# Performance work log

Hardware: AMD Instinct MI355X
Metric: run time of the kernel (lower is better)

Reference implementation:

```python
import jax, jax.numpy as jnp
import numpy as np


def _local_conv2d(x, w, b):
    """Untied (locally connected) conv, stride 1, VALID.
    x: (B, C, H, W); w: (1, O, C, Ho, Wo, k*k); b: (1, O, Ho, Wo) or None.
    Matches torch: x.unfold(2,k).unfold(3,k) -> (B,C,Ho,Wo,k,k) flattened (k*k),
    then (x[:,None] * w).sum([2,-1]) + b.
    """
    B, C, H, W = x.shape
    Ho, Wo = w.shape[3], w.shape[4]
    kh = H - Ho + 1
    kw = W - Wo + 1
    # patches: (B, C*kh*kw, Ho, Wo), feature dim ordered (C, kh, kw) — same as torch unfold
    patches = jax.lax.conv_general_dilated_patches(x, (kh, kw), (1, 1), 'VALID')
    patches = patches.reshape(B, C, kh * kw, Ho, Wo)
    out = jnp.einsum('bckhw,ochwk->bohw', patches, w[0])
    if b is not None:
        out = out + b
    return out


def _maxpool2(x):
    return jax.lax.reduce_window(x, -jnp.inf, jax.lax.max,
                                 (1, 1, 2, 2), (1, 1, 2, 2), 'VALID')


def setup_inputs() -> dict:
    key = jax.random.key(0)
    ks = jax.random.split(key, 11)
    B, C, H, W = 1024, 3, 32, 32
    s = lambda k, shape, fan: jax.random.normal(k, shape, jnp.float32) * np.sqrt(2.0 / fan)
    return {
        'x': jax.random.normal(ks[0], (B, C, H, W), jnp.float32),
        'w1': s(ks[1], (1, 6, 3, 28, 28, 25), 3 * 25),
        'b1': s(ks[2], (1, 6, 28, 28), 28 * 28) ,
        'w2': s(ks[3], (1, 16, 6, 10, 10, 25), 6 * 25),
        'b2': s(ks[4], (1, 16, 10, 10), 10 * 10),
        'w3': s(ks[5], (1, 120, 16, 1, 1, 25), 16 * 25),
        'b3': s(ks[6], (1, 120, 1, 1), 1),
        'fc2_w': s(ks[7], (84, 120), 120),
        'fc2_b': jnp.zeros((84,), jnp.float32),
        'fc3_w': s(ks[8], (10, 84), 84),
        'fc3_b': jnp.zeros((10,), jnp.float32),
    }


def reference(x, w1, b1, w2, b2, w3, b3, fc2_w, fc2_b, fc3_w, fc3_b):
    h = _maxpool2(jax.nn.relu(_local_conv2d(x, w1, b1)))   # (B,6,14,14)
    h = _maxpool2(jax.nn.relu(_local_conv2d(h, w2, b2)))   # (B,16,5,5)
    h = jax.nn.relu(_local_conv2d(h, w3, b3))              # (B,120,1,1)
    h = h.reshape(h.shape[0], -1)                          # (B,120)
    h = jax.nn.relu(h @ fc2_w.T + fc2_b)                   # (B,84)
    return h @ fc3_w.T + fc3_b                             # (B,10)
```

## Files before the change

kernel.cpp:

```cpp
#include <hip/hip_runtime.h>
#include <math.h>

#define NB 1024

__global__ __launch_bounds__(256) void k_transpose(const float* __restrict__ x,
                                                   float* __restrict__ xT) {
  __shared__ float tile[64][65];
  const int c0 = blockIdx.x * 64;
  const int b0 = blockIdx.y * 64;
  const int tx = threadIdx.x & 63;
  const int ty = threadIdx.x >> 6;
#pragma unroll
  for (int r = 0; r < 16; ++r) {
    const int bb = r * 4 + ty;
    tile[bb][tx] = x[(size_t)(b0 + bb) * 3072 + c0 + tx];
  }
  __syncthreads();
#pragma unroll
  for (int r = 0; r < 16; ++r) {
    const int cc = r * 4 + ty;
    xT[(size_t)(c0 + cc) * NB + b0 + tx] = tile[tx][cc];
  }
}

__global__ __launch_bounds__(256) void k_conv1(const float* __restrict__ xT,
                                               const float* __restrict__ w1,
                                               const float* __restrict__ b1,
                                               float* __restrict__ h1) {
  const int pos = blockIdx.x;
  const int ph = pos / 14, pw = pos % 14;
  const int b = blockIdx.y * 256 + threadIdx.x;

  __shared__ __align__(16) float wL[72 * 28];
  __shared__ float bL[24];
  for (int t = threadIdx.x; t < 72 * 25; t += 256) {
    const int chunk = t / 25, p = t - chunk * 25;
    const int o = chunk / 12, rem = chunk - o * 12;
    const int c = rem >> 2, i = (rem >> 1) & 1, j = rem & 1;
    wL[chunk * 28 + p] =
        w1[((size_t)((o * 3 + c) * 28 + (2 * ph + i)) * 28 + (2 * pw + j)) * 25 + p];
  }
  if (threadIdx.x < 24) {
    const int o = threadIdx.x >> 2, i = (threadIdx.x >> 1) & 1, j = threadIdx.x & 1;
    bL[threadIdx.x] = b1[(size_t)(o * 28 + (2 * ph + i)) * 28 + (2 * pw + j)];
  }
  __syncthreads();

  float acc[6][2][2];
#pragma unroll
  for (int o = 0; o < 6; ++o)
#pragma unroll
    for (int i = 0; i < 2; ++i)
#pragma unroll
      for (int j = 0; j < 2; ++j) acc[o][i][j] = 0.f;

  for (int c = 0; c < 3; ++c) {
    float xw[6][6];
#pragma unroll
    for (int dh = 0; dh < 6; ++dh)
#pragma unroll
      for (int dw = 0; dw < 6; ++dw)
        xw[dh][dw] =
            xT[((size_t)(c * 32 + (2 * ph + dh)) * 32 + (2 * pw + dw)) * NB + b];
#pragma unroll
    for (int o = 0; o < 6; ++o)
#pragma unroll
      for (int i = 0; i < 2; ++i)
#pragma unroll
        for (int j = 0; j < 2; ++j) {
          const float* wp = &wL[((o * 3 + c) * 4 + i * 2 + j) * 28];
#pragma unroll
          for (int p = 0; p < 25; ++p)
            acc[o][i][j] = fmaf(xw[i + p / 5][j + p % 5], wp[p], acc[o][i][j]);
        }
  }

#pragma unroll
  for (int o = 0; o < 6; ++o) {
    float v[2][2];
#pragma unroll
    for (int i = 0; i < 2; ++i)
#pragma unroll
      for (int j = 0; j < 2; ++j)
        v[i][j] = fmaxf(acc[o][i][j] + bL[o * 4 + i * 2 + j], 0.f);
    const float m = fmaxf(fmaxf(v[0][0], v[0][1]), fmaxf(v[1][0], v[1][1]));
    h1[((size_t)(o * 14 + ph) * 14 + pw) * NB + b] = m;
  }
}

__global__ __launch_bounds__(256) void k_conv2(const float* __restrict__ h1,
                                               const float* __restrict__ w2,
                                               const float* __restrict__ b2,
                                               float* __restrict__ h2) {
  const int pos = blockIdx.x;
  const int ph = pos / 5, pw = pos - 5 * (pos / 5);
  const int og = blockIdx.y;
  const int b = blockIdx.z * 256 + threadIdx.x;

  __shared__ __align__(16) float wL[96 * 28];
  __shared__ float bL[16];
  for (int t = threadIdx.x; t < 96 * 25; t += 256) {
    const int chunk = t / 25, p = t - chunk * 25;
    const int oo = chunk / 24, rem = chunk - oo * 24;
    const int c = rem >> 2, i = (rem >> 1) & 1, j = rem & 1;
    const int o = og * 4 + oo;
    wL[chunk * 28 + p] =
        w2[((size_t)((o * 6 + c) * 10 + (2 * ph + i)) * 10 + (2 * pw + j)) * 25 + p];
  }
  if (threadIdx.x < 16) {
    const int oo = threadIdx.x >> 2, i = (threadIdx.x >> 1) & 1, j = threadIdx.x & 1;
    const int o = og * 4 + oo;
    bL[threadIdx.x] = b2[(size_t)(o * 10 + (2 * ph + i)) * 10 + (2 * pw + j)];
  }
  __syncthreads();

  float acc[4][2][2];
#pragma unroll
  for (int oo = 0; oo < 4; ++oo)
#pragma unroll
    for (int i = 0; i < 2; ++i)
#pragma unroll
      for (int j = 0; j < 2; ++j) acc[oo][i][j] = 0.f;

  for (int c = 0; c < 6; ++c) {
    float xw[6][6];
#pragma unroll
    for (int dh = 0; dh < 6; ++dh)
#pragma unroll
      for (int dw = 0; dw < 6; ++dw)
        xw[dh][dw] =
            h1[((size_t)(c * 14 + (2 * ph + dh)) * 14 + (2 * pw + dw)) * NB + b];
#pragma unroll
    for (int oo = 0; oo < 4; ++oo)
#pragma unroll
      for (int i = 0; i < 2; ++i)
#pragma unroll
        for (int j = 0; j < 2; ++j) {
          const float* wp = &wL[((oo * 6 + c) * 4 + i * 2 + j) * 28];
#pragma unroll
          for (int p = 0; p < 25; ++p)
            acc[oo][i][j] = fmaf(xw[i + p / 5][j + p % 5], wp[p], acc[oo][i][j]);
        }
  }

#pragma unroll
  for (int oo = 0; oo < 4; ++oo) {
    const int o = og * 4 + oo;
    float v[2][2];
#pragma unroll
    for (int i = 0; i < 2; ++i)
#pragma unroll
      for (int j = 0; j < 2; ++j)
        v[i][j] = fmaxf(acc[oo][i][j] + bL[oo * 4 + i * 2 + j], 0.f);
    const float m = fmaxf(fmaxf(v[0][0], v[0][1]), fmaxf(v[1][0], v[1][1]));
    h2[((size_t)(o * 5 + ph) * 5 + pw) * NB + b] = m;
  }
}

__global__ __launch_bounds__(256) void k_conv3(const float* __restrict__ h2,
                                               const float* __restrict__ w3,
                                               const float* __restrict__ b3,
                                               float* __restrict__ h3) {
  const int o = blockIdx.x;
  const int b = blockIdx.y * 256 + threadIdx.x;
  __shared__ __align__(16) float wL[400];
  for (int t = threadIdx.x; t < 400; t += 256) wL[t] = w3[(size_t)o * 400 + t];
  __syncthreads();

  float a0 = 0.f, a1 = 0.f, a2 = 0.f, a3 = 0.f;
#pragma unroll 8
  for (int k = 0; k < 400; k += 4) {
    a0 = fmaf(h2[(size_t)(k + 0) * NB + b], wL[k + 0], a0);
    a1 = fmaf(h2[(size_t)(k + 1) * NB + b], wL[k + 1], a1);
    a2 = fmaf(h2[(size_t)(k + 2) * NB + b], wL[k + 2], a2);
    a3 = fmaf(h2[(size_t)(k + 3) * NB + b], wL[k + 3], a3);
  }
  h3[(size_t)o * NB + b] = fmaxf((a0 + a1) + (a2 + a3) + b3[o], 0.f);
}

__global__ __launch_bounds__(256) void k_fc2(const float* __restrict__ h3,
                                             const float* __restrict__ fc2w,
                                             const float* __restrict__ fc2b,
                                             float* __restrict__ h4) {
  const int b = blockIdx.x * 64 + (threadIdx.x & 63);
  const int jj = threadIdx.x >> 6;
  const int j = blockIdx.y * 4 + jj;
  __shared__ __align__(16) float wL[4 * 120];
  for (int t = threadIdx.x; t < 480; t += 256)
    wL[t] = fc2w[(size_t)blockIdx.y * 480 + t];
  __syncthreads();

  const float* __restrict__ wp = &wL[jj * 120];
  float a0 = 0.f, a1 = 0.f;
#pragma unroll
  for (int k = 0; k < 120; k += 2) {
    a0 = fmaf(h3[(size_t)(k + 0) * NB + b], wp[k + 0], a0);
    a1 = fmaf(h3[(size_t)(k + 1) * NB + b], wp[k + 1], a1);
  }
  h4[(size_t)j * NB + b] = fmaxf(a0 + a1 + fc2b[j], 0.f);
}

__global__ __launch_bounds__(256) void k_fc3(const float* __restrict__ h4,
                                             const float* __restrict__ fc3w,
                                             const float* __restrict__ fc3b,
                                             float* __restrict__ out) {
  const int b = blockIdx.x * 64 + (threadIdx.x & 63);
  const int ii = threadIdx.x >> 6;
  const int i = blockIdx.y * 4 + ii;
  __shared__ __align__(16) float wL[4 * 84];
  for (int t = threadIdx.x; t < 336; t += 256) {
    const int gi = blockIdx.y * 336 + t;
    wL[t] = (gi < 840) ? fc3w[gi] : 0.f;
  }
  __syncthreads();

  if (i < 10) {
    const float* __restrict__ wp = &wL[ii * 84];
    float a0 = 0.f, a1 = 0.f;
#pragma unroll
    for (int j = 0; j < 84; j += 2) {
      a0 = fmaf(h4[(size_t)(j + 0) * NB + b], wp[j + 0], a0);
      a1 = fmaf(h4[(size_t)(j + 1) * NB + b], wp[j + 1], a1);
    }
    out[(size_t)b * 10 + i] = a0 + a1 + fc3b[i];
  }
}

extern "C" void kernel_launch(void* const* d_in, const int* in_sizes, int n_in,
                              void* d_out, int out_size, void* d_ws, size_t ws_size,
                              hipStream_t stream) {
  const float* x    = (const float*)d_in[0];
  const float* w1   = (const float*)d_in[1];
  const float* b1   = (const float*)d_in[2];
  const float* w2   = (const float*)d_in[3];
  const float* b2   = (const float*)d_in[4];
  const float* w3   = (const float*)d_in[5];
  const float* b3   = (const float*)d_in[6];
  const float* fc2w = (const float*)d_in[7];
  const float* fc2b = (const float*)d_in[8];
  const float* fc3w = (const float*)d_in[9];
  const float* fc3b = (const float*)d_in[10];
  float* out = (float*)d_out;

  float* ws = (float*)d_ws;
  float* xT = ws;
  float* h1 = xT + 3145728;
  float* h2 = h1 + 1204224;
  float* h3 = h2 + 409600;
  float* h4 = xT;

  k_transpose<<<dim3(48, 16), 256, 0, stream>>>(x, xT);
  k_conv1<<<dim3(196, 4), 256, 0, stream>>>(xT, w1, b1, h1);
  k_conv2<<<dim3(25, 4, 4), 256, 0, stream>>>(h1, w2, b2, h2);
  k_conv3<<<dim3(120, 4), 256, 0, stream>>>(h2, w3, b3, h3);
  k_fc2<<<dim3(16, 21), 256, 0, stream>>>(h3, fc2w, fc2b, h4);
  k_fc3<<<dim3(16, 3), 256, 0, stream>>>(h4, fc3w, fc3b, out);
}
```

Measured before the change: 171.4 us.

## Drop input transpose kernel and halve conv2 output-channel group per block

Removes the separate transpose pass. conv1 now reads the original batch-major input directly, using float2 row loads per thread. This saves a full read and write of the input plus one launch. The trade-off is that adjacent threads now load addresses 3072 floats apart, so global loads are no longer coalesced and depend on cache reuse across blocks. Separately, conv2 now computes 2 output channels per block instead of 4, which doubles the grid to improve occupancy at the cost of reloading input windows more often.

Result: slower. 175.9 us (+2.7%).

```diff
diff --git a/kernel.cpp b/kernel.cpp
--- a/kernel.cpp
+++ b/kernel.cpp
@@ -3,27 +3,7 @@
 
 #define NB 1024
 
-__global__ __launch_bounds__(256) void k_transpose(const float* __restrict__ x,
-                                                   float* __restrict__ xT) {
-  __shared__ float tile[64][65];
-  const int c0 = blockIdx.x * 64;
-  const int b0 = blockIdx.y * 64;
-  const int tx = threadIdx.x & 63;
-  const int ty = threadIdx.x >> 6;
-#pragma unroll
-  for (int r = 0; r < 16; ++r) {
-    const int bb = r * 4 + ty;
-    tile[bb][tx] = x[(size_t)(b0 + bb) * 3072 + c0 + tx];
-  }
-  __syncthreads();
-#pragma unroll
-  for (int r = 0; r < 16; ++r) {
-    const int cc = r * 4 + ty;
-    xT[(size_t)(c0 + cc) * NB + b0 + tx] = tile[tx][cc];
-  }
-}
-
-__global__ __launch_bounds__(256) void k_conv1(const float* __restrict__ xT,
+__global__ __launch_bounds__(256) void k_conv1(const float* __restrict__ x,
                                                const float* __restrict__ w1,
                                                const float* __restrict__ b1,
                                                float* __restrict__ h1) {
@@ -57,11 +37,15 @@
   for (int c = 0; c < 3; ++c) {
     float xw[6][6];
 #pragma unroll
-    for (int dh = 0; dh < 6; ++dh)
-#pragma unroll
-      for (int dw = 0; dw < 6; ++dw)
-        xw[dh][dw] =
-            xT[((size_t)(c * 32 + (2 * ph + dh)) * 32 + (2 * pw + dw)) * NB + b];
+    for (int dh = 0; dh < 6; ++dh) {
+      const float* row = x + (size_t)b * 3072 + c * 1024 + (2 * ph + dh) * 32 + 2 * pw;
+      const float2 r0 = *reinterpret_cast<const float2*>(row + 0);
+      const float2 r1 = *reinterpret_cast<const float2*>(row + 2);
+      const float2 r2 = *reinterpret_cast<const float2*>(row + 4);
+      xw[dh][0] = r0.x; xw[dh][1] = r0.y;
+      xw[dh][2] = r1.x; xw[dh][3] = r1.y;
+      xw[dh][4] = r2.x; xw[dh][5] = r2.y;
+    }
 #pragma unroll
     for (int o = 0; o < 6; ++o)
 #pragma unroll
@@ -93,30 +77,30 @@
                                                const float* __restrict__ b2,
                                                float* __restrict__ h2) {
   const int pos = blockIdx.x;
-  const int ph = pos / 5, pw = pos - 5 * (pos / 5);
+  const int ph = pos / 5, pw = pos % 5;
   const int og = blockIdx.y;
   const int b = blockIdx.z * 256 + threadIdx.x;
 
-  __shared__ __align__(16) float wL[96 * 28];
-  __shared__ float bL[16];
-  for (int t = threadIdx.x; t < 96 * 25; t += 256) {
+  __shared__ __align__(16) float wL[48 * 28];
+  __shared__ float bL[8];
+  for (int t = threadIdx.x; t < 48 * 25; t += 256) {
     const int chunk = t / 25, p = t - chunk * 25;
     const int oo = chunk / 24, rem = chunk - oo * 24;
     const int c = rem >> 2, i = (rem >> 1) & 1, j = rem & 1;
-    const int o = og * 4 + oo;
+    const int o = og * 2 + oo;
     wL[chunk * 28 + p] =
         w2[((size_t)((o * 6 + c) * 10 + (2 * ph + i)) * 10 + (2 * pw + j)) * 25 + p];
   }
-  if (threadIdx.x < 16) {
+  if (threadIdx.x < 8) {
     const int oo = threadIdx.x >> 2, i = (threadIdx.x >> 1) & 1, j = threadIdx.x & 1;
-    const int o = og * 4 + oo;
+    const int o = og * 2 + oo;
     bL[threadIdx.x] = b2[(size_t)(o * 10 + (2 * ph + i)) * 10 + (2 * pw + j)];
   }
   __syncthreads();
 
-  float acc[4][2][2];
-#pragma unroll
-  for (int oo = 0; oo < 4; ++oo)
+  float acc[2][2][2];
+#pragma unroll
+  for (int oo = 0; oo < 2; ++oo)
 #pragma unroll
     for (int i = 0; i < 2; ++i)
 #pragma unroll
@@ -131,7 +115,7 @@
         xw[dh][dw] =
             h1[((size_t)(c * 14 + (2 * ph + dh)) * 14 + (2 * pw + dw)) * NB + b];
 #pragma unroll
-    for (int oo = 0; oo < 4; ++oo)
+    for (int oo = 0; oo < 2; ++oo)
 #pragma unroll
       for (int i = 0; i < 2; ++i)
 #pragma unroll
@@ -144,8 +128,8 @@
   }
 
 #pragma unroll
-  for (int oo = 0; oo < 4; ++oo) {
-    const int o = og * 4 + oo;
+  for (int oo = 0; oo < 2; ++oo) {
+    const int o = og * 2 + oo;
     float v[2][2];
 #pragma unroll
     for (int i = 0; i < 2; ++i)
@@ -243,15 +227,13 @@
   float* out = (float*)d_out;
 
   float* ws = (float*)d_ws;
-  float* xT = ws;
-  float* h1 = xT + 3145728;
+  float* h1 = ws;
   float* h2 = h1 + 1204224;
   float* h3 = h2 + 409600;
-  float* h4 = xT;
-
-  k_transpose<<<dim3(48, 16), 256, 0, stream>>>(x, xT);
-  k_conv1<<<dim3(196, 4), 256, 0, stream>>>(xT, w1, b1, h1);
-  k_conv2<<<dim3(25, 4, 4), 256, 0, stream>>>(h1, w2, b2, h2);
+  float* h4 = h3 + 122880;
+
+  k_conv1<<<dim3(196, 4), 256, 0, stream>>>(x, w1, b1, h1);
+  k_conv2<<<dim3(25, 8, 4), 256, 0, stream>>>(h1, w2, b2, h2);
   k_conv3<<<dim3(120, 4), 256, 0, stream>>>(h2, w3, b3, h3);
   k_fc2<<<dim3(16, 21), 256, 0, stream>>>(h3, fc2w, fc2b, h4);
   k_fc3<<<dim3(16, 3), 256, 0, stream>>>(h4, fc3w, fc3b, out);
```
